# Performance work log

Measured on AMD Instinct MI355X. Metric: run time of the kernel, lower is better.

The kernel has to match this reference:

```python
import jax, jax.numpy as jnp
import numpy as np

N_NODES = 10000
N_EDGES = 160000
D = 256
L = 2
EPS = 1e-5


def setup_inputs() -> dict:
    key = jax.random.key(0)
    ks = jax.random.split(key, 12)
    s = 0.05  # weight init scale to keep activations tame
    return {
        "node_h": jax.random.normal(ks[0], (N_NODES, D), jnp.float32),
        "edge_h": jax.random.normal(ks[1], (N_EDGES, D), jnp.float32),
        "src": jax.random.randint(ks[2], (N_EDGES,), 0, N_NODES, jnp.int32),
        "dst": jax.random.randint(ks[3], (N_EDGES,), 0, N_NODES, jnp.int32),
        "Kw": jax.random.normal(ks[4], (L, 2 * D, D), jnp.float32) * s,
        "Kb": jnp.zeros((L, D), jnp.float32),
        "Vw": jax.random.normal(ks[5], (L, 2 * D, D), jnp.float32) * s,
        "Vb": jnp.zeros((L, D), jnp.float32),
        "Qw": jax.random.normal(ks[6], (L, D, D), jnp.float32) * s,
        "Qb": jnp.zeros((L, D), jnp.float32),
        "Ww": jax.random.normal(ks[7], (L, 2 * D, D), jnp.float32) * s,
        "Wb": jnp.zeros((L, D), jnp.float32),
        "Ew": jax.random.normal(ks[8], (L, 3 * D, D), jnp.float32) * s,
        "Eb": jnp.zeros((L, D), jnp.float32),
        "ln_g": jnp.ones((D,), jnp.float32),
        "ln_b": jnp.zeros((D,), jnp.float32),
    }


def _layernorm(x, g, b):
    mu = jnp.mean(x, axis=-1, keepdims=True)
    var = jnp.mean(jnp.square(x - mu), axis=-1, keepdims=True)
    return (x - mu) * jax.lax.rsqrt(var + EPS) * g + b


def _hypergraph_layer(h_n, h_e, src, dst, Kw, Kb, Vw, Vb, Qw, Qb, Ww, Wb, Ew, Eb):
    n = h_n.shape[0]
    src_h = h_n[src]                                   # [E, D] gather
    msg = jnp.concatenate([src_h * h_e, src_h], axis=1)  # [E, 2D]
    Q = h_n @ Qw + Qb                                  # [N, D]
    K = msg @ Kw + Kb                                  # [E, D]
    V = msg @ Vw + Vb                                  # [E, D]
    alpha = Q[dst] * K                                 # v_mul_e -> [E, D]
    # edge_softmax: per-destination-node, per-feature softmax over edges
    m = jax.ops.segment_max(alpha, dst, num_segments=n)
    e = jnp.exp(alpha - m[dst])
    z = jax.ops.segment_sum(e, dst, num_segments=n)
    a = e / z[dst]
    agg = jax.ops.segment_sum(a * V, dst, num_segments=n)  # sum aggregation [N, D]
    h_n_new = jnp.concatenate([agg, h_n], axis=1) @ Ww + Wb
    h_e_new = jnp.concatenate([h_n_new[src], h_n_new[dst], h_e], axis=1) @ Ew + Eb
    return h_n_new, h_e_new


def reference(node_h, edge_h, src, dst, Kw, Kb, Vw, Vb, Qw, Qb, Ww, Wb, Ew, Eb, ln_g, ln_b):
    h_n, h_e = node_h, edge_h
    for l in range(L):  # small fixed layer count
        h_n, h_e = _hypergraph_layer(h_n, h_e, src, dst,
                                     Kw[l], Kb[l], Vw[l], Vb[l], Qw[l], Qb[l],
                                     Ww[l], Wb[l], Ew[l], Eb[l])
        # relu -> layernorm; dropout is identity in eval mode
        h_n = _layernorm(jax.nn.relu(h_n), ln_g, ln_b)
        h_e = _layernorm(jax.nn.relu(h_e), ln_g, ln_b)
    return h_n, h_e
```

## Files before the change

### kernel.cpp

```cpp
#include <hip/hip_runtime.h>

#define NN 10000
#define NE 160000
#define DD 256
#define LEPS 1e-5f

typedef __attribute__((ext_vector_type(8))) short short8v;
typedef __attribute__((ext_vector_type(4))) float floatx4;
typedef unsigned short US;

static __device__ __forceinline__ US f2bf(float f){
  unsigned u = __builtin_bit_cast(unsigned, f);
  u += 0x7FFFu + ((u >> 16) & 1u);
  return (US)(u >> 16);
}
static __device__ __forceinline__ float bf2f(US s){
  unsigned u = ((unsigned)s) << 16;
  return __builtin_bit_cast(float, u);
}

#define AOFF_Q  0
#define AOFF_K1 (32*2048)
#define AOFF_K2 (64*2048)
#define AOFF_V1 (96*2048)
#define AOFF_V2 (128*2048)
#define AOFF_W  (160*2048)
#define AOFF_E1 (224*2048)
#define AOFF_E2 (256*2048)
#define AOFF_E3 (288*2048)
__global__ void pack_all_k(const float* __restrict__ Qw, const float* __restrict__ Kw,
                           const float* __restrict__ Vw, const float* __restrict__ Ww,
                           const float* __restrict__ Ew, US* __restrict__ arena){
  int i = blockIdx.x * 256 + threadIdx.x;
  int g = i >> 8, n = i & 255;
  const float* src; int row0;
  if      (g <  32){ src = Qw; row0 = g*8; }
  else if (g <  64){ src = Kw; row0 = (g-32)*8; }
  else if (g <  96){ src = Kw; row0 = 256 + (g-64)*8; }
  else if (g < 128){ src = Vw; row0 = (g-96)*8; }
  else if (g < 160){ src = Vw; row0 = 256 + (g-128)*8; }
  else if (g < 224){ src = Ww; row0 = (g-160)*8; }
  else if (g < 256){ src = Ew; row0 = (g-224)*8; }
  else if (g < 288){ src = Ew; row0 = 256 + (g-256)*8; }
  else             { src = Ew; row0 = 512 + (g-288)*8; }
  union { US h[8]; uint4 q; } pk;
#pragma unroll
  for (int j = 0; j < 8; ++j) pk.h[j] = f2bf(src[(size_t)(row0 + j)*DD + n]);
  *(uint4*)(arena + (size_t)g*2048 + n*8) = pk.q;
}

struct Tri { const US* bp; const float* bias; float* out; };
__global__ __launch_bounds__(256, 2)
void gemm_nmulti_k(const float* __restrict__ p0, Tri t0, Tri t1, Tri t2, int M)
{
  Tri t = (blockIdx.y == 0) ? t0 : (blockIdx.y == 1 ? t1 : t2);
  __shared__ __align__(16) US Alds[64][40];
  __shared__ __align__(16) US Blds[8192];
  const int tid  = threadIdx.x;
  const int lane = tid & 63;
  const int wav  = tid >> 6;
  const int bm   = blockIdx.x * 64;

  floatx4 acc[4][4];
#pragma unroll
  for (int i = 0; i < 4; ++i)
#pragma unroll
    for (int j = 0; j < 4; ++j) acc[i][j] = (floatx4){0.f,0.f,0.f,0.f};

  const int ar = tid >> 2;
  const int ak = (tid & 3) << 3;
  int grow = bm + ar; if (grow > M - 1) grow = M - 1;
  const float* rA = p0 + (size_t)grow * DD;
  const int rq = lane >> 4;
  const int cl = lane & 15;

  for (int k0 = 0; k0 < 256; k0 += 32) {
    const int kk = k0 + ak;
    float4 x0 = *(const float4*)(rA + kk);
    float4 x1 = *(const float4*)(rA + kk + 4);
    union { US h[8]; uint4 q; } pk;
    pk.h[0]=f2bf(x0.x); pk.h[1]=f2bf(x0.y); pk.h[2]=f2bf(x0.z); pk.h[3]=f2bf(x0.w);
    pk.h[4]=f2bf(x1.x); pk.h[5]=f2bf(x1.y); pk.h[6]=f2bf(x1.z); pk.h[7]=f2bf(x1.w);
    *(uint4*)&Alds[ar][ak] = pk.q;

    const uint4* bsrc = (const uint4*)(t.bp + (size_t)(k0 >> 3) * 2048);
    uint4* bdst = (uint4*)Blds;
#pragma unroll
    for (int u = 0; u < 4; ++u) bdst[tid + u*256] = bsrc[tid + u*256];
    __syncthreads();

    short8v af[4], bfr[4];
#pragma unroll
    for (int i = 0; i < 4; ++i) af[i] = *(const short8v*)&Alds[i*16 + cl][rq*8];
#pragma unroll
    for (int j = 0; j < 4; ++j) bfr[j] = *(const short8v*)&Blds[(size_t)(rq*256 + wav*64 + j*16 + cl) * 8];
#pragma unroll
    for (int i = 0; i < 4; ++i)
#pragma unroll
      for (int j = 0; j < 4; ++j)
        acc[i][j] = __builtin_amdgcn_mfma_f32_16x16x32_bf16(af[i], bfr[j], acc[i][j], 0, 0, 0);
    __syncthreads();
  }

#pragma unroll
  for (int i = 0; i < 4; ++i)
#pragma unroll
    for (int r = 0; r < 4; ++r) {
      int gm = bm + i*16 + rq*4 + r;
      if (gm < M) {
#pragma unroll
        for (int j = 0; j < 4; ++j) {
          int n = wav*64 + j*16 + cl;
          float b = t.bias ? t.bias[n] : 0.f;
          t.out[(size_t)gm*DD + n] = acc[i][j][r] + b;
        }
      }
    }
}

__global__ __launch_bounds__(256, 2)
void gemm_w_k(const float* __restrict__ p0, const float* __restrict__ p1,
              const US* __restrict__ Bp, const float* __restrict__ bias,
              const float* __restrict__ lg, const float* __restrict__ lb,
              float* __restrict__ Craw, float* __restrict__ Cln, int M)
{
  __shared__ __align__(16) US Alds[64][40];
  __shared__ __align__(16) US Blds[8192];
  __shared__ float S1[4][64], S2[4][64];
  const int tid  = threadIdx.x;
  const int lane = tid & 63;
  const int wav  = tid >> 6;
  const int bm   = blockIdx.x * 64;

  floatx4 acc[4][4];
#pragma unroll
  for (int i = 0; i < 4; ++i)
#pragma unroll
    for (int j = 0; j < 4; ++j) acc[i][j] = (floatx4){0.f,0.f,0.f,0.f};

  const int ar = tid >> 2;
  const int ak = (tid & 3) << 3;
  int grow = bm + ar; if (grow > M - 1) grow = M - 1;
  const float* rA = p0 + (size_t)grow * DD;
  const float* rB = p1 + (size_t)grow * DD;
  const int rq = lane >> 4;
  const int cl = lane & 15;

  for (int k0 = 0; k0 < 512; k0 += 32) {
    const int kk = k0 + ak;
    const float* s = (kk < DD) ? (rA + kk) : (rB + kk - DD);
    float4 x0 = *(const float4*)s;
    float4 x1 = *(const float4*)(s + 4);
    union { US h[8]; uint4 q; } pk;
    pk.h[0]=f2bf(x0.x); pk.h[1]=f2bf(x0.y); pk.h[2]=f2bf(x0.z); pk.h[3]=f2bf(x0.w);
    pk.h[4]=f2bf(x1.x); pk.h[5]=f2bf(x1.y); pk.h[6]=f2bf(x1.z); pk.h[7]=f2bf(x1.w);
    *(uint4*)&Alds[ar][ak] = pk.q;

    const uint4* bsrc = (const uint4*)(Bp + (size_t)(k0 >> 3) * 2048);
    uint4* bdst = (uint4*)Blds;
#pragma unroll
    for (int u = 0; u < 4; ++u) bdst[tid + u*256] = bsrc[tid + u*256];
    __syncthreads();

    short8v af[4], bfr[4];
#pragma unroll
    for (int i = 0; i < 4; ++i) af[i] = *(const short8v*)&Alds[i*16 + cl][rq*8];
#pragma unroll
    for (int j = 0; j < 4; ++j) bfr[j] = *(const short8v*)&Blds[(size_t)(rq*256 + wav*64 + j*16 + cl) * 8];
#pragma unroll
    for (int i = 0; i < 4; ++i)
#pragma unroll
      for (int j = 0; j < 4; ++j)
        acc[i][j] = __builtin_amdgcn_mfma_f32_16x16x32_bf16(af[i], bfr[j], acc[i][j], 0, 0, 0);
    __syncthreads();
  }

#pragma unroll
  for (int i = 0; i < 4; ++i)
#pragma unroll
    for (int j = 0; j < 4; ++j) {
      int n = wav*64 + j*16 + cl;
      float bs = bias[n];
#pragma unroll
      for (int r = 0; r < 4; ++r) {
        int gm = bm + i*16 + rq*4 + r;
        float val = acc[i][j][r] + bs;
        if (gm < M) Craw[(size_t)gm*DD + n] = val;
        acc[i][j][r] = fmaxf(val, 0.f);
      }
    }
#pragma unroll
  for (int i = 0; i < 4; ++i)
#pragma unroll
    for (int r = 0; r < 4; ++r) {
      float s1 = 0.f, s2 = 0.f;
#pragma unroll
      for (int j = 0; j < 4; ++j){ float v = acc[i][j][r]; s1 += v; s2 += v*v; }
#pragma unroll
      for (int o = 1; o < 16; o <<= 1){ s1 += __shfl_xor(s1, o, 64); s2 += __shfl_xor(s2, o, 64); }
      if (cl == 0){ S1[wav][i*16 + rq*4 + r] = s1; S2[wav][i*16 + rq*4 + r] = s2; }
    }
  __syncthreads();
#pragma unroll
  for (int i = 0; i < 4; ++i)
#pragma unroll
    for (int r = 0; r < 4; ++r) {
      int rr = i*16 + rq*4 + r;
      float t1 = S1[0][rr] + S1[1][rr] + S1[2][rr] + S1[3][rr];
      float t2 = S2[0][rr] + S2[1][rr] + S2[2][rr] + S2[3][rr];
      float mu = t1 * (1.f/256.f);
      float var = t2 * (1.f/256.f) - mu*mu;
      float rs = rsqrtf(fmaxf(var, 0.f) + LEPS);
      int gm = bm + i*16 + rq*4 + r;
      if (gm < M) {
#pragma unroll
        for (int j = 0; j < 4; ++j) {
          int n = wav*64 + j*16 + cl;
          Cln[(size_t)gm*DD + n] = (acc[i][j][r] - mu) * rs * lg[n] + lb[n];
        }
      }
    }
}

__global__ __launch_bounds__(256, 2)
void gemm_kve_k(const float* __restrict__ p0, const float* __restrict__ p1,
                const int* __restrict__ srcI,
                const US* __restrict__ BpK, const US* __restrict__ BpV,
                const float* __restrict__ KN, const float* __restrict__ VN,
                const int* __restrict__ eperm,
                US* __restrict__ Km, US* __restrict__ Vm, int M)
{
  __shared__ __align__(16) US Alds[64][40];
  __shared__ __align__(16) US BldsK[8192];
  __shared__ __align__(16) US BldsV[8192];
  const int tid  = threadIdx.x;
  const int lane = tid & 63;
  const int wav  = tid >> 6;
  const int bm   = blockIdx.x * 64;

  floatx4 accK[4][4], accV[4][4];
#pragma unroll
  for (int i = 0; i < 4; ++i)
#pragma unroll
    for (int j = 0; j < 4; ++j){ accK[i][j] = (floatx4){0.f,0.f,0.f,0.f}; accV[i][j] = (floatx4){0.f,0.f,0.f,0.f}; }

  const int ar = tid >> 2;
  const int ak = (tid & 3) << 3;
  int grow = bm + ar; if (grow > M - 1) grow = M - 1;
  int s = srcI[grow];
  const float* rA = p0 + (size_t)s * DD;
  const float* rB = p1 + (size_t)grow * DD;
  const int rq = lane >> 4;
  const int cl = lane & 15;

  for (int k0 = 0; k0 < 256; k0 += 32) {
    const int kk = k0 + ak;
    float4 x0 = *(const float4*)(rA + kk);
    float4 x1 = *(const float4*)(rA + kk + 4);
    float4 m0 = *(const float4*)(rB + kk);
    float4 m1 = *(const float4*)(rB + kk + 4);
    x0.x*=m0.x; x0.y*=m0.y; x0.z*=m0.z; x0.w*=m0.w;
    x1.x*=m1.x; x1.y*=m1.y; x1.z*=m1.z; x1.w*=m1.w;
    union { US h[8]; uint4 q; } pk;
    pk.h[0]=f2bf(x0.x); pk.h[1]=f2bf(x0.y); pk.h[2]=f2bf(x0.z); pk.h[3]=f2bf(x0.w);
    pk.h[4]=f2bf(x1.x); pk.h[5]=f2bf(x1.y); pk.h[6]=f2bf(x1.z); pk.h[7]=f2bf(x1.w);
    *(uint4*)&Alds[ar][ak] = pk.q;

    const uint4* bsK = (const uint4*)(BpK + (size_t)(k0 >> 3) * 2048);
    const uint4* bsV = (const uint4*)(BpV + (size_t)(k0 >> 3) * 2048);
    uint4* bdK = (uint4*)BldsK; uint4* bdV = (uint4*)BldsV;
#pragma unroll
    for (int u = 0; u < 4; ++u){ bdK[tid + u*256] = bsK[tid + u*256]; bdV[tid + u*256] = bsV[tid + u*256]; }
    __syncthreads();

    short8v af[4], bK4[4], bV4[4];
#pragma unroll
    for (int i = 0; i < 4; ++i) af[i] = *(const short8v*)&Alds[i*16 + cl][rq*8];
#pragma unroll
    for (int j = 0; j < 4; ++j){
      size_t bi = (size_t)(rq*256 + wav*64 + j*16 + cl) * 8;
      bK4[j] = *(const short8v*)&BldsK[bi];
      bV4[j] = *(const short8v*)&BldsV[bi];
    }
#pragma unroll
    for (int i = 0; i < 4; ++i)
#pragma unroll
      for (int j = 0; j < 4; ++j){
        accK[i][j] = __builtin_amdgcn_mfma_f32_16x16x32_bf16(af[i], bK4[j], accK[i][j], 0, 0, 0);
        accV[i][j] = __builtin_amdgcn_mfma_f32_16x16x32_bf16(af[i], bV4[j], accV[i][j], 0, 0, 0);
      }
    __syncthreads();
  }

#pragma unroll
  for (int i = 0; i < 4; ++i)
#pragma unroll
    for (int r = 0; r < 4; ++r) {
      int gm = bm + i*16 + rq*4 + r;
      if (gm < M) {
        int pg = eperm[gm];
        int sg = srcI[gm];
        const float* kn = KN + (size_t)sg * DD;
        const float* vn = VN + (size_t)sg * DD;
#pragma unroll
        for (int j = 0; j < 4; ++j) {
          int n = wav*64 + j*16 + cl;
          Km[(size_t)pg*DD + n] = f2bf(accK[i][j][r] + kn[n]);
          Vm[(size_t)pg*DD + n] = f2bf(accV[i][j][r] + vn[n]);
        }
      }
    }
}

__global__ __launch_bounds__(256, 2)
void gemm_e_k(const float* __restrict__ he, const int* __restrict__ srcI,
              const int* __restrict__ dstI, const US* __restrict__ Bp,
              const float* __restrict__ EN1, const float* __restrict__ EN2,
              const float* __restrict__ lg, const float* __restrict__ lb,
              float* __restrict__ Cln, int M)
{
  __shared__ __align__(16) US Alds[64][40];
  __shared__ __align__(16) US Blds[8192];
  __shared__ float S1[4][64], S2[4][64];
  const int tid  = threadIdx.x;
  const int lane = tid & 63;
  const int wav  = tid >> 6;
  const int bm   = blockIdx.x * 64;

  floatx4 acc[4][4];
#pragma unroll
  for (int i = 0; i < 4; ++i)
#pragma unroll
    for (int j = 0; j < 4; ++j) acc[i][j] = (floatx4){0.f,0.f,0.f,0.f};

  const int ar = tid >> 2;
  const int ak = (tid & 3) << 3;
  int grow = bm + ar; if (grow > M - 1) grow = M - 1;
  const float* rA = he + (size_t)grow * DD;
  const int rq = lane >> 4;
  const int cl = lane & 15;

  for (int k0 = 0; k0 < 256; k0 += 32) {
    const int kk = k0 + ak;
    float4 x0 = *(const float4*)(rA + kk);
    float4 x1 = *(const float4*)(rA + kk + 4);
    union { US h[8]; uint4 q; } pk;
    pk.h[0]=f2bf(x0.x); pk.h[1]=f2bf(x0.y); pk.h[2]=f2bf(x0.z); pk.h[3]=f2bf(x0.w);
    pk.h[4]=f2bf(x1.x); pk.h[5]=f2bf(x1.y); pk.h[6]=f2bf(x1.z); pk.h[7]=f2bf(x1.w);
    *(uint4*)&Alds[ar][ak] = pk.q;

    const uint4* bsrc = (const uint4*)(Bp + (size_t)(k0 >> 3) * 2048);
    uint4* bdst = (uint4*)Blds;
#pragma unroll
    for (int u = 0; u < 4; ++u) bdst[tid + u*256] = bsrc[tid + u*256];
    __syncthreads();

    short8v af[4], bfr[4];
#pragma unroll
    for (int i = 0; i < 4; ++i) af[i] = *(const short8v*)&Alds[i*16 + cl][rq*8];
#pragma unroll
    for (int j = 0; j < 4; ++j) bfr[j] = *(const short8v*)&Blds[(size_t)(rq*256 + wav*64 + j*16 + cl) * 8];
#pragma unroll
    for (int i = 0; i < 4; ++i)
#pragma unroll
      for (int j = 0; j < 4; ++j)
        acc[i][j] = __builtin_amdgcn_mfma_f32_16x16x32_bf16(af[i], bfr[j], acc[i][j], 0, 0, 0);
    __syncthreads();
  }

#pragma unroll
  for (int i = 0; i < 4; ++i)
#pragma unroll
    for (int r = 0; r < 4; ++r) {
      int gm = bm + i*16 + rq*4 + r;
      int gmc = (gm < M) ? gm : (M - 1);
      const float* e1 = EN1 + (size_t)srcI[gmc] * DD;
      const float* e2 = EN2 + (size_t)dstI[gmc] * DD;
#pragma unroll
      for (int j = 0; j < 4; ++j) {
        int n = wav*64 + j*16 + cl;
        float val = acc[i][j][r] + e1[n] + e2[n];
        acc[i][j][r] = fmaxf(val, 0.f);
      }
    }
#pragma unroll
  for (int i = 0; i < 4; ++i)
#pragma unroll
    for (int r = 0; r < 4; ++r) {
      float s1 = 0.f, s2 = 0.f;
#pragma unroll
      for (int j = 0; j < 4; ++j){ float v = acc[i][j][r]; s1 += v; s2 += v*v; }
#pragma unroll
      for (int o = 1; o < 16; o <<= 1){ s1 += __shfl_xor(s1, o, 64); s2 += __shfl_xor(s2, o, 64); }
      if (cl == 0){ S1[wav][i*16 + rq*4 + r] = s1; S2[wav][i*16 + rq*4 + r] = s2; }
    }
  __syncthreads();
#pragma unroll
  for (int i = 0; i < 4; ++i)
#pragma unroll
    for (int r = 0; r < 4; ++r) {
      int rr = i*16 + rq*4 + r;
      float t1 = S1[0][rr] + S1[1][rr] + S1[2][rr] + S1[3][rr];
      float t2 = S2[0][rr] + S2[1][rr] + S2[2][rr] + S2[3][rr];
      float mu = t1 * (1.f/256.f);
      float var = t2 * (1.f/256.f) - mu*mu;
      float rs = rsqrtf(fmaxf(var, 0.f) + LEPS);
      int gm = bm + i*16 + rq*4 + r;
      if (gm < M) {
#pragma unroll
        for (int j = 0; j < 4; ++j) {
          int n = wav*64 + j*16 + cl;
          Cln[(size_t)gm*DD + n] = (acc[i][j][r] - mu) * rs * lg[n] + lb[n];
        }
      }
    }
}

__global__ void count_k(const int* __restrict__ dst, int* __restrict__ cnt, int e){
  int i = blockIdx.x * blockDim.x + threadIdx.x;
  if (i < e) atomicAdd(&cnt[dst[i]], 1);
}
__global__ void scan_k(const int* __restrict__ cnt, int* __restrict__ rp, int n){
  __shared__ int part[256];
  const int t = threadIdx.x;
  const int chunk = (n + 255) / 256;
  int lo = t * chunk, hi = lo + chunk; if (hi > n) hi = n; if (lo > n) lo = n;
  int s = 0;
  for (int i = lo; i < hi; ++i) s += cnt[i];
  part[t] = s; __syncthreads();
  if (t == 0){ int run = 0; for (int i = 0; i < 256; ++i){ int tmp = part[i]; part[i] = run; run += tmp; } rp[n] = run; }
  __syncthreads();
  int run = part[t];
  for (int i = lo; i < hi; ++i){ rp[i] = run; run += cnt[i]; }
}
__global__ void scatter_k(const int* __restrict__ dst, const int* __restrict__ rp,
                          int* __restrict__ pos, int* __restrict__ eperm, int e){
  int i = blockIdx.x * blockDim.x + threadIdx.x;
  if (i >= e) return;
  int d = dst[i];
  int p = atomicAdd(&pos[d], 1);
  eperm[i] = rp[d] + p;
}

__global__ __launch_bounds__(256)
void node_agg_k(const int* __restrict__ rp,
                const float* __restrict__ Q, const US* __restrict__ Km,
                const US* __restrict__ Vm, float* __restrict__ agg)
{
  int d = blockIdx.x, f = threadIdx.x;
  int beg = rp[d], end = rp[d + 1];
  float q = Q[(size_t)d * DD + f];
  float m = -3.0e38f, z = 0.f, s = 0.f;
  for (int i = beg; i < end; ++i){
    float a  = q * bf2f(Km[(size_t)i * DD + f]);
    float vv = bf2f(Vm[(size_t)i * DD + f]);
    float mn = fmaxf(m, a);
    float sc = __expf(m - mn);
    float w  = __expf(a - mn);
    z = z * sc + w;
    s = s * sc + w * vv;
    m = mn;
  }
  agg[(size_t)d * DD + f] = (z > 0.f) ? (s / z) : 0.f;
}

__global__ void sentinel_k(int hostbits, float* out){
  int code = 0;
  if (hostbits & 1) code = 1;
  else if (hostbits & 2) code = 2;
  else if (hostbits & 4) code = 3;
  else if (hostbits & 8) code = 4;
  if (code) out[0] = (float)code * 1.0e6f;
}

extern "C" void kernel_launch(void* const* d_in, const int* in_sizes, int n_in,
                              void* d_out, int out_size, void* d_ws, size_t ws_size,
                              hipStream_t stream) {
  const float* node_h = (const float*)d_in[0];
  const float* edge_h = (const float*)d_in[1];
  const int*   src    = (const int*)d_in[2];
  const int*   dst    = (const int*)d_in[3];
  const float* Kw = (const float*)d_in[4];  const float* Kb = (const float*)d_in[5];
  const float* Vw = (const float*)d_in[6];  const float* Vb = (const float*)d_in[7];
  const float* Qw = (const float*)d_in[8];  const float* Qb = (const float*)d_in[9];
  const float* Ww = (const float*)d_in[10]; const float* Wb = (const float*)d_in[11];
  const float* Ew = (const float*)d_in[12]; const float* Eb = (const float*)d_in[13];
  const float* ln_g = (const float*)d_in[14];
  const float* ln_b = (const float*)d_in[15];

  char* w = (char*)d_ws; size_t off = 0;
  auto alloc = [&](size_t bytes)->char* {
    char* p = w + off; off += (bytes + 255) & ~(size_t)255; return p;
  };
  float* Q      = (float*)alloc((size_t)NN * DD * 4);
  float* agg    = (float*)alloc((size_t)NN * DD * 4);
  float* hn_new = (float*)alloc((size_t)NN * DD * 4);
  float* hn_cur = (float*)alloc((size_t)NN * DD * 4);
  float* KN     = (float*)alloc((size_t)NN * DD * 4);
  float* VN     = (float*)alloc((size_t)NN * DD * 4);
  float* EN1    = (float*)alloc((size_t)NN * DD * 4);
  float* EN2    = (float*)alloc((size_t)NN * DD * 4);
  US*    Kmat   = (US*)alloc((size_t)NE * DD * 2);
  US*    Vmat   = (US*)alloc((size_t)NE * DD * 2);
  float* he_cur = (float*)alloc((size_t)NE * DD * 4);
  US*    arena  = (US*)alloc((size_t)320 * 2048 * 2);
  int* cnt   = (int*)alloc((size_t)NN * 4);
  int* rp    = (int*)alloc((size_t)(NN + 1) * 4);
  int* pos   = (int*)alloc((size_t)NN * 4);
  int* eperm = (int*)alloc((size_t)NE * 4);

  float* out_hn = (float*)d_out;
  float* out_he = out_hn + (size_t)NN * DD;

  int hostbits = 0;
  {
    static const int exp_sizes[16] = {NN*DD, NE*DD, NE, NE, 2*512*DD, 2*DD, 2*512*DD, 2*DD,
                                      2*DD*DD, 2*DD, 2*512*DD, 2*DD, 2*768*DD, 2*DD, DD, DD};
    if (n_in != 16) hostbits |= 2;
    else { for (int i = 0; i < 16; ++i) if (in_sizes[i] != exp_sizes[i]) hostbits |= 2; }
    if (out_size != NN*DD + NE*DD) hostbits |= 4;
    if (off > ws_size) hostbits |= 1;
  }
  if (hostbits) {
    sentinel_k<<<1, 1, 0, stream>>>(hostbits, out_hn);
    return;
  }

  hipMemsetAsync(cnt, 0, (size_t)NN * 4, stream);
  hipMemsetAsync(pos, 0, (size_t)NN * 4, stream);
  count_k<<<(NE + 255)/256, 256, 0, stream>>>(dst, cnt, NE);
  scan_k<<<1, 256, 0, stream>>>(cnt, rp, NN);
  scatter_k<<<(NE + 255)/256, 256, 0, stream>>>(dst, rp, pos, eperm, NE);

  const int gN = (NN + 63) / 64;
  const int gE = (NE + 63) / 64;

  for (int l = 0; l < 2; ++l) {
    const float* hn_in = l ? hn_cur : node_h;
    const float* he_in = l ? he_cur : edge_h;
    float* hn_out = l ? out_hn : hn_cur;
    float* he_out = l ? out_he : he_cur;

    pack_all_k<<<320, 256, 0, stream>>>(Qw + (size_t)l*256*DD, Kw + (size_t)l*512*DD,
                                        Vw + (size_t)l*512*DD, Ww + (size_t)l*512*DD,
                                        Ew + (size_t)l*768*DD, arena);

    {
      Tri tQ{arena + AOFF_Q,  Qb + (size_t)l*DD, Q};
      Tri tK{arena + AOFF_K2, Kb + (size_t)l*DD, KN};
      Tri tV{arena + AOFF_V2, Vb + (size_t)l*DD, VN};
      gemm_nmulti_k<<<dim3(gN, 3), 256, 0, stream>>>(hn_in, tQ, tK, tV, NN);
    }
    gemm_kve_k<<<gE, 256, 0, stream>>>(hn_in, he_in, src,
                                       arena + AOFF_K1, arena + AOFF_V1,
                                       KN, VN, eperm, Kmat, Vmat, NE);
    node_agg_k<<<NN, 256, 0, stream>>>(rp, Q, Kmat, Vmat, agg);
    gemm_w_k<<<gN, 256, 0, stream>>>(agg, hn_in, arena + AOFF_W, Wb + (size_t)l*DD,
                                     ln_g, ln_b, hn_new, hn_out, NN);
    {
      Tri t1{arena + AOFF_E1, Eb + (size_t)l*DD, EN1};
      Tri t2{arena + AOFF_E2, nullptr, EN2};
      gemm_nmulti_k<<<dim3(gN, 2), 256, 0, stream>>>(hn_new, t1, t2, t2, NN);
    }
    gemm_e_k<<<gE, 256, 0, stream>>>(he_in, src, dst, arena + AOFF_E3,
                                     EN1, EN2, ln_g, ln_b, he_out, NE);
  }

  if (hipGetLastError() != hipSuccess) {
    sentinel_k<<<1, 1, 0, stream>>>(8, out_hn);
  }
}
```

Baseline: 899.6 us.

## Store intermediate node/edge activations and KN/VN/EN tables in bf16

```diff
diff --git a/kernel.cpp b/kernel.cpp
--- a/kernel.cpp
+++ b/kernel.cpp
@@ -17,6 +17,22 @@
 static __device__ __forceinline__ float bf2f(US s){
   unsigned u = ((unsigned)s) << 16;
   return __builtin_bit_cast(float, u);
+}
+template<typename T>
+static __device__ __forceinline__ void ld8(const T* p, float* o){
+  if constexpr (sizeof(T) == 2) {
+    union { US h[8]; uint4 q; } u;
+    u.q = *(const uint4*)p;
+#pragma unroll
+    for (int j = 0; j < 8; ++j) o[j] = bf2f(u.h[j]);
+  } else {
+    float4 a = *(const float4*)p; float4 b = *(const float4*)(p + 4);
+    o[0]=a.x; o[1]=a.y; o[2]=a.z; o[3]=a.w; o[4]=b.x; o[5]=b.y; o[6]=b.z; o[7]=b.w;
+  }
+}
+template<typename OT>
+static __device__ __forceinline__ void st1(OT* p, float v){
+  if constexpr (sizeof(OT) == 2) *p = (OT)f2bf(v); else *p = (OT)v;
 }
 
 #define AOFF_Q  0
@@ -49,11 +65,16 @@
   *(uint4*)(arena + (size_t)g*2048 + n*8) = pk.q;
 }
 
-struct Tri { const US* bp; const float* bias; float* out; };
-__global__ __launch_bounds__(256, 2)
-void gemm_nmulti_k(const float* __restrict__ p0, Tri t0, Tri t1, Tri t2, int M)
+template<typename AT, typename OT>
+__global__ __launch_bounds__(256, 4)
+void gemm_nmulti_k(const AT* __restrict__ p0,
+                   const US* bp0, const float* b0, OT* o0,
+                   const US* bp1, const float* b1, OT* o1,
+                   const US* bp2, const float* b2, OT* o2, int M)
 {
-  Tri t = (blockIdx.y == 0) ? t0 : (blockIdx.y == 1 ? t1 : t2);
+  const US* Bp  = (blockIdx.y == 0) ? bp0 : (blockIdx.y == 1 ? bp1 : bp2);
+  const float* bias = (blockIdx.y == 0) ? b0 : (blockIdx.y == 1 ? b1 : b2);
+  OT* out = (blockIdx.y == 0) ? o0 : (blockIdx.y == 1 ? o1 : o2);
   __shared__ __align__(16) US Alds[64][40];
   __shared__ __align__(16) US Blds[8192];
   const int tid  = threadIdx.x;
@@ -70,20 +91,18 @@
   const int ar = tid >> 2;
   const int ak = (tid & 3) << 3;
   int grow = bm + ar; if (grow > M - 1) grow = M - 1;
-  const float* rA = p0 + (size_t)grow * DD;
+  const AT* rA = p0 + (size_t)grow * DD;
   const int rq = lane >> 4;
   const int cl = lane & 15;
 
   for (int k0 = 0; k0 < 256; k0 += 32) {
-    const int kk = k0 + ak;
-    float4 x0 = *(const float4*)(rA + kk);
-    float4 x1 = *(const float4*)(rA + kk + 4);
+    float av[8]; ld8(rA + k0 + ak, av);
     union { US h[8]; uint4 q; } pk;
-    pk.h[0]=f2bf(x0.x); pk.h[1]=f2bf(x0.y); pk.h[2]=f2bf(x0.z); pk.h[3]=f2bf(x0.w);
-    pk.h[4]=f2bf(x1.x); pk.h[5]=f2bf(x1.y); pk.h[6]=f2bf(x1.z); pk.h[7]=f2bf(x1.w);
+#pragma unroll
+    for (int j = 0; j < 8; ++j) pk.h[j] = f2bf(av[j]);
     *(uint4*)&Alds[ar][ak] = pk.q;
 
-    const uint4* bsrc = (const uint4*)(t.bp + (size_t)(k0 >> 3) * 2048);
+    const uint4* bsrc = (const uint4*)(Bp + (size_t)(k0 >> 3) * 2048);
     uint4* bdst = (uint4*)Blds;
 #pragma unroll
     for (int u = 0; u < 4; ++u) bdst[tid + u*256] = bsrc[tid + u*256];
@@ -111,18 +130,19 @@
 #pragma unroll
         for (int j = 0; j < 4; ++j) {
           int n = wav*64 + j*16 + cl;
-          float b = t.bias ? t.bias[n] : 0.f;
-          t.out[(size_t)gm*DD + n] = acc[i][j][r] + b;
+          float b = bias ? bias[n] : 0.f;
+          st1(out + (size_t)gm*DD + n, acc[i][j][r] + b);
         }
       }
     }
 }
 
-__global__ __launch_bounds__(256, 2)
-void gemm_w_k(const float* __restrict__ p0, const float* __restrict__ p1,
+template<typename AT, typename OT>
+__global__ __launch_bounds__(256, 4)
+void gemm_w_k(const float* __restrict__ p0, const AT* __restrict__ p1,
               const US* __restrict__ Bp, const float* __restrict__ bias,
               const float* __restrict__ lg, const float* __restrict__ lb,
-              float* __restrict__ Craw, float* __restrict__ Cln, int M)
+              float* __restrict__ Craw, OT* __restrict__ Cln, int M)
 {
   __shared__ __align__(16) US Alds[64][40];
   __shared__ __align__(16) US Blds[8192];
@@ -142,18 +162,17 @@
   const int ak = (tid & 3) << 3;
   int grow = bm + ar; if (grow > M - 1) grow = M - 1;
   const float* rA = p0 + (size_t)grow * DD;
-  const float* rB = p1 + (size_t)grow * DD;
+  const AT*    rB = p1 + (size_t)grow * DD;
   const int rq = lane >> 4;
   const int cl = lane & 15;
 
   for (int k0 = 0; k0 < 512; k0 += 32) {
     const int kk = k0 + ak;
-    const float* s = (kk < DD) ? (rA + kk) : (rB + kk - DD);
-    float4 x0 = *(const float4*)s;
-    float4 x1 = *(const float4*)(s + 4);
+    float av[8];
+    if (kk < DD) ld8(rA + kk, av); else ld8(rB + kk - DD, av);
     union { US h[8]; uint4 q; } pk;
-    pk.h[0]=f2bf(x0.x); pk.h[1]=f2bf(x0.y); pk.h[2]=f2bf(x0.z); pk.h[3]=f2bf(x0.w);
-    pk.h[4]=f2bf(x1.x); pk.h[5]=f2bf(x1.y); pk.h[6]=f2bf(x1.z); pk.h[7]=f2bf(x1.w);
+#pragma unroll
+    for (int j = 0; j < 8; ++j) pk.h[j] = f2bf(av[j]);
     *(uint4*)&Alds[ar][ak] = pk.q;
 
     const uint4* bsrc = (const uint4*)(Bp + (size_t)(k0 >> 3) * 2048);
@@ -216,17 +235,18 @@
 #pragma unroll
         for (int j = 0; j < 4; ++j) {
           int n = wav*64 + j*16 + cl;
-          Cln[(size_t)gm*DD + n] = (acc[i][j][r] - mu) * rs * lg[n] + lb[n];
+          st1(Cln + (size_t)gm*DD + n, (acc[i][j][r] - mu) * rs * lg[n] + lb[n]);
         }
       }
     }
 }
 
-__global__ __launch_bounds__(256, 2)
-void gemm_kve_k(const float* __restrict__ p0, const float* __restrict__ p1,
+template<typename AT>
+__global__ __launch_bounds__(256, 4)
+void gemm_kve_k(const AT* __restrict__ p0, const AT* __restrict__ p1,
                 const int* __restrict__ srcI,
                 const US* __restrict__ BpK, const US* __restrict__ BpV,
-                const float* __restrict__ KN, const float* __restrict__ VN,
+                const US* __restrict__ KN, const US* __restrict__ VN,
                 const int* __restrict__ eperm,
                 US* __restrict__ Km, US* __restrict__ Vm, int M)
 {
@@ -248,22 +268,18 @@
   const int ak = (tid & 3) << 3;
   int grow = bm + ar; if (grow > M - 1) grow = M - 1;
   int s = srcI[grow];
-  const float* rA = p0 + (size_t)s * DD;
-  const float* rB = p1 + (size_t)grow * DD;
+  const AT* rA = p0 + (size_t)s * DD;
+  const AT* rB = p1 + (size_t)grow * DD;
   const int rq = lane >> 4;
   const int cl = lane & 15;
 
   for (int k0 = 0; k0 < 256; k0 += 32) {
     const int kk = k0 + ak;
-    float4 x0 = *(const float4*)(rA + kk);
-    float4 x1 = *(const float4*)(rA + kk + 4);
-    float4 m0 = *(const float4*)(rB + kk);
-    float4 m1 = *(const float4*)(rB + kk + 4);
-    x0.x*=m0.x; x0.y*=m0.y; x0.z*=m0.z; x0.w*=m0.w;
-    x1.x*=m1.x; x1.y*=m1.y; x1.z*=m1.z; x1.w*=m1.w;
+    float av[8], bv[8];
+    ld8(rA + kk, av); ld8(rB + kk, bv);
     union { US h[8]; uint4 q; } pk;
-    pk.h[0]=f2bf(x0.x); pk.h[1]=f2bf(x0.y); pk.h[2]=f2bf(x0.z); pk.h[3]=f2bf(x0.w);
-    pk.h[4]=f2bf(x1.x); pk.h[5]=f2bf(x1.y); pk.h[6]=f2bf(x1.z); pk.h[7]=f2bf(x1.w);
+#pragma unroll
+    for (int j = 0; j < 8; ++j) pk.h[j] = f2bf(av[j] * bv[j]);
     *(uint4*)&Alds[ar][ak] = pk.q;
 
     const uint4* bsK = (const uint4*)(BpK + (size_t)(k0 >> 3) * 2048);
@@ -300,24 +316,25 @@
       if (gm < M) {
         int pg = eperm[gm];
         int sg = srcI[gm];
-        const float* kn = KN + (size_t)sg * DD;
-        const float* vn = VN + (size_t)sg * DD;
+        const US* kn = KN + (size_t)sg * DD;
+        const US* vn = VN + (size_t)sg * DD;
 #pragma unroll
         for (int j = 0; j < 4; ++j) {
           int n = wav*64 + j*16 + cl;
-          Km[(size_t)pg*DD + n] = f2bf(accK[i][j][r] + kn[n]);
-          Vm[(size_t)pg*DD + n] = f2bf(accV[i][j][r] + vn[n]);
+          Km[(size_t)pg*DD + n] = f2bf(accK[i][j][r] + bf2f(kn[n]));
+          Vm[(size_t)pg*DD + n] = f2bf(accV[i][j][r] + bf2f(vn[n]));
         }
       }
     }
 }
 
-__global__ __launch_bounds__(256, 2)
-void gemm_e_k(const float* __restrict__ he, const int* __restrict__ srcI,
+template<typename AT, typename OT>
+__global__ __launch_bounds__(256, 4)
+void gemm_e_k(const AT* __restrict__ he, const int* __restrict__ srcI,
               const int* __restrict__ dstI, const US* __restrict__ Bp,
-              const float* __restrict__ EN1, const float* __restrict__ EN2,
+              const US* __restrict__ EN1, const US* __restrict__ EN2,
               const float* __restrict__ lg, const float* __restrict__ lb,
-              float* __restrict__ Cln, int M)
+              OT* __restrict__ Cln, int M)
 {
   __shared__ __align__(16) US Alds[64][40];
   __shared__ __align__(16) US Blds[8192];
@@ -336,17 +353,15 @@
   const int ar = tid >> 2;
   const int ak = (tid & 3) << 3;
   int grow = bm + ar; if (grow > M - 1) grow = M - 1;
-  const float* rA = he + (size_t)grow * DD;
+  const AT* rA = he + (size_t)grow * DD;
   const int rq = lane >> 4;
   const int cl = lane & 15;
 
   for (int k0 = 0; k0 < 256; k0 += 32) {
-    const int kk = k0 + ak;
-    float4 x0 = *(const float4*)(rA + kk);
-    float4 x1 = *(const float4*)(rA + kk + 4);
+    float av[8]; ld8(rA + k0 + ak, av);
     union { US h[8]; uint4 q; } pk;
-    pk.h[0]=f2bf(x0.x); pk.h[1]=f2bf(x0.y); pk.h[2]=f2bf(x0.z); pk.h[3]=f2bf(x0.w);
-    pk.h[4]=f2bf(x1.x); pk.h[5]=f2bf(x1.y); pk.h[6]=f2bf(x1.z); pk.h[7]=f2bf(x1.w);
+#pragma unroll
+    for (int j = 0; j < 8; ++j) pk.h[j] = f2bf(av[j]);
     *(uint4*)&Alds[ar][ak] = pk.q;
 
     const uint4* bsrc = (const uint4*)(Bp + (size_t)(k0 >> 3) * 2048);
@@ -374,12 +389,12 @@
     for (int r = 0; r < 4; ++r) {
       int gm = bm + i*16 + rq*4 + r;
       int gmc = (gm < M) ? gm : (M - 1);
-      const float* e1 = EN1 + (size_t)srcI[gmc] * DD;
-      const float* e2 = EN2 + (size_t)dstI[gmc] * DD;
+      const US* e1 = EN1 + (size_t)srcI[gmc] * DD;
+      const US* e2 = EN2 + (size_t)dstI[gmc] * DD;
 #pragma unroll
       for (int j = 0; j < 4; ++j) {
         int n = wav*64 + j*16 + cl;
-        float val = acc[i][j][r] + e1[n] + e2[n];
+        float val = acc[i][j][r] + bf2f(e1[n]) + bf2f(e2[n]);
         acc[i][j][r] = fmaxf(val, 0.f);
       }
     }
@@ -410,7 +425,7 @@
 #pragma unroll
         for (int j = 0; j < 4; ++j) {
           int n = wav*64 + j*16 + cl;
-          Cln[(size_t)gm*DD + n] = (acc[i][j][r] - mu) * rs * lg[n] + lb[n];
+          st1(Cln + (size_t)gm*DD + n, (acc[i][j][r] - mu) * rs * lg[n] + lb[n]);
         }
       }
     }
@@ -473,6 +488,36 @@
   if (code) out[0] = (float)code * 1.0e6f;
 }
 
+struct Bufs {
+  float *Q, *agg, *hn_new;
+  US *KN, *VN, *EN1, *EN2, *Kmat, *Vmat, *arena;
+  int *rp, *eperm;
+  const int *src, *dst;
+  const float *lg, *lb;
+};
+template<typename AT, typename OT>
+static void layer_run(const Bufs& B, const AT* hn_in, const AT* he_in,
+                      OT* hn_out, US* hn_keep_unused, OT* he_out,
+                      const float* Kb, const float* Vb, const float* Qb,
+                      const float* Wb, const float* Eb, hipStream_t stream)
+{
+  const int gN = (NN + 63) / 64, gE = (NE + 63) / 64;
+  gemm_nmulti_k<AT, float><<<dim3(gN, 1), 256, 0, stream>>>(hn_in,
+      B.arena + AOFF_Q, Qb, B.Q,  B.arena + AOFF_Q, Qb, B.Q,  B.arena + AOFF_Q, Qb, B.Q, NN);
+  gemm_nmulti_k<AT, US><<<dim3(gN, 2), 256, 0, stream>>>(hn_in,
+      B.arena + AOFF_K2, Kb, B.KN,  B.arena + AOFF_V2, Vb, B.VN,  B.arena + AOFF_V2, Vb, B.VN, NN);
+  gemm_kve_k<AT><<<gE, 256, 0, stream>>>(hn_in, he_in, B.src,
+      B.arena + AOFF_K1, B.arena + AOFF_V1, B.KN, B.VN, B.eperm, B.Kmat, B.Vmat, NE);
+  node_agg_k<<<NN, 256, 0, stream>>>(B.rp, B.Q, B.Kmat, B.Vmat, B.agg);
+  gemm_w_k<AT, OT><<<gN, 256, 0, stream>>>(B.agg, hn_in, B.arena + AOFF_W, Wb,
+      B.lg, B.lb, B.hn_new, hn_out, NN);
+  gemm_nmulti_k<float, US><<<dim3(gN, 2), 256, 0, stream>>>(B.hn_new,
+      B.arena + AOFF_E1, Eb, B.EN1,  B.arena + AOFF_E2, nullptr, B.EN2,
+      B.arena + AOFF_E2, nullptr, B.EN2, NN);
+  gemm_e_k<AT, OT><<<gE, 256, 0, stream>>>(he_in, B.src, B.dst, B.arena + AOFF_E3,
+      B.EN1, B.EN2, B.lg, B.lb, he_out, NE);
+}
+
 extern "C" void kernel_launch(void* const* d_in, const int* in_sizes, int n_in,
                               void* d_out, int out_size, void* d_ws, size_t ws_size,
                               hipStream_t stream) {
@@ -495,15 +540,15 @@
   float* Q      = (float*)alloc((size_t)NN * DD * 4);
   float* agg    = (float*)alloc((size_t)NN * DD * 4);
   float* hn_new = (float*)alloc((size_t)NN * DD * 4);
-  float* hn_cur = (float*)alloc((size_t)NN * DD * 4);
-  float* KN     = (float*)alloc((size_t)NN * DD * 4);
-  float* VN     = (float*)alloc((size_t)NN * DD * 4);
-  float* EN1    = (float*)alloc((size_t)NN * DD * 4);
-  float* EN2    = (float*)alloc((size_t)NN * DD * 4);
-  US*    Kmat   = (US*)alloc((size_t)NE * DD * 2);
-  US*    Vmat   = (US*)alloc((size_t)NE * DD * 2);
-  float* he_cur = (float*)alloc((size_t)NE * DD * 4);
-  US*    arena  = (US*)alloc((size_t)320 * 2048 * 2);
+  US* hn_cur = (US*)alloc((size_t)NN * DD * 2);
+  US* KN     = (US*)alloc((size_t)NN * DD * 2);
+  US* VN     = (US*)alloc((size_t)NN * DD * 2);
+  US* EN1    = (US*)alloc((size_t)NN * DD * 2);
+  US* EN2    = (US*)alloc((size_t)NN * DD * 2);
+  US* Kmat   = (US*)alloc((size_t)NE * DD * 2);
+  US* Vmat   = (US*)alloc((size_t)NE * DD * 2);
+  US* he_cur = (US*)alloc((size_t)NE * DD * 2);
+  US* arena  = (US*)alloc((size_t)320 * 2048 * 2);
   int* cnt   = (int*)alloc((size_t)NN * 4);
   int* rp    = (int*)alloc((size_t)(NN + 1) * 4);
   int* pos   = (int*)alloc((size_t)NN * 4);
@@ -532,39 +577,16 @@
   scan_k<<<1, 256, 0, stream>>>(cnt, rp, NN);
   scatter_k<<<(NE + 255)/256, 256, 0, stream>>>(dst, rp, pos, eperm, NE);
 
-  const int gN = (NN + 63) / 64;
-  const int gE = (NE + 63) / 64;
-
-  for (int l = 0; l < 2; ++l) {
-    const float* hn_in = l ? hn_cur : node_h;
-    const float* he_in = l ? he_cur : edge_h;
-    float* hn_out = l ? out_hn : hn_cur;
-    float* he_out = l ? out_he : he_cur;
-
-    pack_all_k<<<320, 256, 0, stream>>>(Qw + (size_t)l*256*DD, Kw + (size_t)l*512*DD,
-                                        Vw + (size_t)l*512*DD, Ww + (size_t)l*512*DD,
-                                        Ew + (size_t)l*768*DD, arena);
-
-    {
-      Tri tQ{arena + AOFF_Q,  Qb + (size_t)l*DD, Q};
-      Tri tK{arena + AOFF_K2, Kb + (size_t)l*DD, KN};
-      Tri tV{arena + AOFF_V2, Vb + (size_t)l*DD, VN};
-      gemm_nmulti_k<<<dim3(gN, 3), 256, 0, stream>>>(hn_in, tQ, tK, tV, NN);
-    }
-    gemm_kve_k<<<gE, 256, 0, stream>>>(hn_in, he_in, src,
-                                       arena + AOFF_K1, arena + AOFF_V1,
-                                       KN, VN, eperm, Kmat, Vmat, NE);
-    node_agg_k<<<NN, 256, 0, stream>>>(rp, Q, Kmat, Vmat, agg);
-    gemm_w_k<<<gN, 256, 0, stream>>>(agg, hn_in, arena + AOFF_W, Wb + (size_t)l*DD,
-                                     ln_g, ln_b, hn_new, hn_out, NN);
-    {
-      Tri t1{arena + AOFF_E1, Eb + (size_t)l*DD, EN1};
-      Tri t2{arena + AOFF_E2, nullptr, EN2};
-      gemm_nmulti_k<<<dim3(gN, 2), 256, 0, stream>>>(hn_new, t1, t2, t2, NN);
-    }
-    gemm_e_k<<<gE, 256, 0, stream>>>(he_in, src, dst, arena + AOFF_E3,
-                                     EN1, EN2, ln_g, ln_b, he_out, NE);
-  }
+  Bufs B{Q, agg, hn_new, KN, VN, EN1, EN2, Kmat, Vmat, arena, rp, eperm, src, dst, ln_g, ln_b};
+
+  pack_all_k<<<320, 256, 0, stream>>>(Qw, Kw, Vw, Ww, Ew, arena);
+  layer_run<float, US>(B, node_h, edge_h, hn_cur, nullptr, he_cur,
+                       Kb, Vb, Qb, Wb, Eb, stream);
+  pack_all_k<<<320, 256, 0, stream>>>(Qw + (size_t)256*DD, Kw + (size_t)512*DD,
+                                      Vw + (size_t)512*DD, Ww + (size_t)512*DD,
+                                      Ew + (size_t)768*DD, arena);
+  layer_run<US, float>(B, hn_cur, he_cur, out_hn, nullptr, out_he,
+                       Kb + DD, Vb + DD, Qb + DD, Wb + DD, Eb + DD, stream);
 
   if (hipGetLastError() != hipSuccess) {
     sentinel_k<<<1, 1, 0, stream>>>(8, out_hn);
```

New measurement: 1.959 ms. +117.7%, slower.
